# Optimization experiments

Hardware: AMD Instinct MI355X
Metric: run time of the kernel (lower is better)

## Reference

```python
import jax, jax.numpy as jnp
import numpy as np

N, E, L, H, C, F, NCLASS, NGRAPH = 50000, 800000, 3, 2, 64, 128, 10, 64
NEG_SLOPE = 0.2


def setup_inputs() -> dict:
    key = jax.random.key(0)
    ks = jax.random.split(key, 8)
    x = jax.random.normal(ks[0], (N, F), dtype=jnp.float32)
    edge_index = jax.random.randint(ks[1], (2, E), 0, N, dtype=jnp.int64)
    batch = jnp.sort(jax.random.randint(ks[2], (N,), 0, NGRAPH, dtype=jnp.int64))
    s = 1.0 / np.sqrt(F)
    W = jax.random.normal(ks[3], (L, F, H * C), dtype=jnp.float32) * s
    att_src = jax.random.normal(ks[4], (L, H, C), dtype=jnp.float32) * s
    att_dst = jax.random.normal(ks[5], (L, H, C), dtype=jnp.float32) * s
    bias = jnp.zeros((L, H * C), dtype=jnp.float32)
    lin_w = jax.random.normal(ks[6], (H * C, NCLASS), dtype=jnp.float32) * s
    lin_b = jnp.zeros((NCLASS,), dtype=jnp.float32)
    return {"x": x, "edge_index": edge_index, "batch": batch, "W": W,
            "att_src": att_src, "att_dst": att_dst, "bias": bias,
            "lin_w": lin_w, "lin_b": lin_b}


def _gat_layer(x, src, dst, w, a_s, a_d, b):
    n = x.shape[0]
    h = (x @ w).reshape(n, H, C)                      # [N,H,C]
    alpha_src = jnp.sum(h * a_s, axis=-1)             # [N,H]
    alpha_dst = jnp.sum(h * a_d, axis=-1)             # [N,H]
    e = jax.nn.leaky_relu(alpha_src[src] + alpha_dst[dst], NEG_SLOPE)  # [E2,H]
    # scatter-softmax over incoming edges of each destination node
    m = jax.ops.segment_max(e, dst, num_segments=n)
    p = jnp.exp(e - m[dst])
    z = jax.ops.segment_sum(p, dst, num_segments=n)
    alpha = p / z[dst]                                # [E2,H]
    msg = h[src] * alpha[:, :, None]                  # [E2,H,C]
    out = jax.ops.segment_sum(msg, dst, num_segments=n)  # [N,H,C]
    return out.reshape(n, H * C) + b


def reference(x, edge_index, batch, W, att_src, att_dst, bias, lin_w, lin_b):
    n = x.shape[0]
    # PyG GATConv default: add self-loops
    loop = jnp.arange(n, dtype=edge_index.dtype)
    src = jnp.concatenate([edge_index[0], loop])
    dst = jnp.concatenate([edge_index[1], loop])
    for l in range(L):
        x = _gat_layer(x, src, dst, W[l], att_src[l], att_dst[l], bias[l])
        x = jax.nn.elu(x)  # activation; dropout/bn inactive (eval, use_bn=False)
    # global mean pool per graph
    sums = jax.ops.segment_sum(x, batch, num_segments=NGRAPH)
    cnt = jax.ops.segment_sum(jnp.ones((n,), x.dtype), batch, num_segments=NGRAPH)
    pooled = sums / jnp.maximum(cnt, 1.0)[:, None]    # [NGRAPH, H*C]
    logits = pooled @ lin_w + lin_b
    return jax.nn.softmax(logits, axis=1)
```

## Files before the change

### kernel.cpp

```cpp
#include <hip/hip_runtime.h>
#include <math.h>

#define NNODES 50000
#define NEDGES 800000
#define NLAYERS 3
#define NHEADS 2
#define NCH 64
#define FDIM 128
#define NCLS 10
#define NGRAPH 64
#define NEG_SLOPE 0.2f
#define GEMMB ((NNODES + 63) / 64)
#define NB 391
#define RADB 391
#define SCN (NB * RADB)
#define NS1 ((SCN + 511) / 512)
#define PCH 8

#define WAVE_SYNC()                      \
  do {                                   \
    __builtin_amdgcn_wave_barrier();     \
    __asm__ volatile("" ::: "memory");   \
  } while (0)

typedef __attribute__((ext_vector_type(8))) short bf16x8;
typedef __attribute__((ext_vector_type(4))) float f32x4;

__device__ __forceinline__ unsigned short f2bf(float f) {
  unsigned int u = __builtin_bit_cast(unsigned int, f);
  unsigned int r = u + 0x7FFFu + ((u >> 16) & 1u);
  return (unsigned short)(r >> 16);
}
__device__ __forceinline__ float bflo(unsigned v) {
  return __builtin_bit_cast(float, v << 16);
}
__device__ __forceinline__ float bfhi(unsigned v) {
  return __builtin_bit_cast(float, v & 0xFFFF0000u);
}

__global__ __launch_bounds__(256) void k_wprep(const float* __restrict__ W,
                                               unsigned* __restrict__ Wt) {
  __shared__ float Lt[128][132];
  int l = blockIdx.x;
  const float* Wl = W + (size_t)l * FDIM * FDIM;
  unsigned* Wtl = Wt + (size_t)l * FDIM * FDIM / 2;
  int t = threadIdx.x;
#pragma unroll
  for (int i = 0; i < 16; ++i) {
    int k = (t >> 5) + 8 * i;
    int n4 = (t & 31) * 4;
    float4 v = *(const float4*)(Wl + (size_t)k * 128 + n4);
    Lt[k][n4 + 0] = v.x;
    Lt[k][n4 + 1] = v.y;
    Lt[k][n4 + 2] = v.z;
    Lt[k][n4 + 3] = v.w;
  }
  __syncthreads();
  int n = t >> 1;
  int kh = (t & 1) * 64;
  for (int kk = 0; kk < 64; kk += 2) {
    unsigned pk = (unsigned)f2bf(Lt[kh + kk][n]) |
                  ((unsigned)f2bf(Lt[kh + kk + 1][n]) << 16);
    Wtl[n * 64 + (kh >> 1) + (kk >> 1)] = pk;
  }
}

__global__ __launch_bounds__(128) void k_goff(const int* __restrict__ batch,
                                              int* __restrict__ goff,
                                              float* __restrict__ gsum) {
  int t = threadIdx.x;
  if (t < NGRAPH) {
    int lo = 0, hi = NNODES;
    while (lo < hi) {
      int mid = (lo + hi) >> 1;
      if (batch[mid] < t) lo = mid + 1;
      else hi = mid;
    }
    goff[t] = lo;
  }
  if (t == 0) goff[NGRAPH] = NNODES;
  for (int i = t; i < NGRAPH * FDIM; i += 128) gsum[i] = 0.f;
}

__device__ __forceinline__ void gemm_body(int blk, const float* __restrict__ X,
                                          const unsigned* __restrict__ Wt,
                                          const float* __restrict__ a_sL,
                                          const float* __restrict__ a_dL,
                                          unsigned* __restrict__ Hb,
                                          float* __restrict__ as_,
                                          float* __restrict__ ad_) {
  int t = threadIdx.x;
  int lane = t & 63;
  int w = t >> 6;
  int row0 = blk * 64;
  int n16 = lane & 15;
  int quad = lane >> 4;
  int m0 = w * 16;

  int gr = row0 + m0 + n16;
  const float* xp = X + (size_t)min(gr, NNODES - 1) * 128;

  f32x4 acc[8];
#pragma unroll
  for (int nt = 0; nt < 8; ++nt) {
    f32x4 z = {0.f, 0.f, 0.f, 0.f};
    acc[nt] = z;
  }
#pragma unroll
  for (int kk = 0; kk < 4; ++kk) {
    float4 va = *(const float4*)(xp + kk * 32 + quad * 8);
    float4 vb = *(const float4*)(xp + kk * 32 + quad * 8 + 4);
    bf16x8 af;
    af[0] = (short)f2bf(va.x); af[1] = (short)f2bf(va.y);
    af[2] = (short)f2bf(va.z); af[3] = (short)f2bf(va.w);
    af[4] = (short)f2bf(vb.x); af[5] = (short)f2bf(vb.y);
    af[6] = (short)f2bf(vb.z); af[7] = (short)f2bf(vb.w);
#pragma unroll
    for (int nt = 0; nt < 8; ++nt) {
      bf16x8 bf = *(const bf16x8*)(Wt + (size_t)(nt * 16 + n16) * 64 +
                                   kk * 16 + quad * 4);
      acc[nt] =
          __builtin_amdgcn_mfma_f32_16x16x32_bf16(af, bf, acc[nt], 0, 0, 0);
    }
  }

  float asv[8], adv[8];
#pragma unroll
  for (int nt = 0; nt < 8; ++nt) {
    asv[nt] = a_sL[nt * 16 + n16];
    adv[nt] = a_dL[nt * 16 + n16];
  }
#pragma unroll
  for (int r = 0; r < 4; ++r) {
    int row = row0 + m0 + quad * 4 + r;
    bool ok = (row < NNODES);
    float ps0 = 0.f, pd0 = 0.f, ps1 = 0.f, pd1 = 0.f;
#pragma unroll
    for (int nt = 0; nt < 4; ++nt) {
      ps0 += acc[nt][r] * asv[nt];
      pd0 += acc[nt][r] * adv[nt];
      ps1 += acc[nt + 4][r] * asv[nt + 4];
      pd1 += acc[nt + 4][r] * adv[nt + 4];
    }
#pragma unroll
    for (int off = 1; off < 16; off <<= 1) {
      ps0 += __shfl_xor(ps0, off, 64);
      pd0 += __shfl_xor(pd0, off, 64);
      ps1 += __shfl_xor(ps1, off, 64);
      pd1 += __shfl_xor(pd1, off, 64);
    }
    if (ok && n16 == 0) {
      as_[row * 2 + 0] = ps0;
      as_[row * 2 + 1] = ps1;
      ad_[row * 2 + 0] = pd0;
      ad_[row * 2 + 1] = pd1;
    }
    if (ok) {
#pragma unroll
      for (int nt = 0; nt < 4; ++nt) {
        unsigned pk = (unsigned)f2bf(acc[nt][r]) |
                      ((unsigned)f2bf(acc[nt + 4][r]) << 16);
        Hb[(size_t)row * 64 + nt * 16 + n16] = pk;
      }
    }
  }
}

__global__ __launch_bounds__(256) void k_gemm(const float* __restrict__ X,
                                              const unsigned* __restrict__ Wt,
                                              const float* __restrict__ a_sL,
                                              const float* __restrict__ a_dL,
                                              unsigned* __restrict__ Hb,
                                              float* __restrict__ as_,
                                              float* __restrict__ ad_) {
  gemm_body(blockIdx.x, X, Wt, a_sL, a_dL, Hb, as_, ad_);
}

__global__ __launch_bounds__(256) void k_front(
    const float* __restrict__ X, const unsigned* __restrict__ Wt,
    const float* __restrict__ a_sL, const float* __restrict__ a_dL,
    unsigned* __restrict__ Hb, float* __restrict__ as_,
    float* __restrict__ ad_, const int* __restrict__ ei,
    int* __restrict__ bh) {
  int b = blockIdx.x;
  if (b < GEMMB) {
    gemm_body(b, X, Wt, a_sL, a_dL, Hb, as_, ad_);
  } else {
    __shared__ int hist[NB];
    int blk = b - GEMMB;
    int t = threadIdx.x;
    for (int i = t; i < NB; i += 256) hist[i] = 0;
    __syncthreads();
    int e0 = blk * 2048;
#pragma unroll
    for (int i = 0; i < 8; ++i) {
      int e = e0 + i * 256 + t;
      if (e < NEDGES) atomicAdd(&hist[ei[NEDGES + e] >> 7], 1);
    }
    __syncthreads();
    for (int i = t; i < NB; i += 256) bh[i * RADB + blk] = hist[i];
  }
}

__global__ __launch_bounds__(256) void k_s1(int* __restrict__ sc,
                                            int* __restrict__ bpart) {
  __shared__ int ps[256];
  int t = threadIdx.x;
  int f0 = blockIdx.x * 512 + 2 * t;
  int x0 = (f0 < SCN) ? sc[f0] : 0;
  int x1 = (f0 + 1 < SCN) ? sc[f0 + 1] : 0;
  int pair = x0 + x1;
  ps[t] = pair;
  __syncthreads();
  for (int off = 1; off < 256; off <<= 1) {
    int v = (t >= off) ? ps[t - off] : 0;
    __syncthreads();
    ps[t] += v;
    __syncthreads();
  }
  int ex = ps[t] - pair;
  if (f0 < SCN) sc[f0] = ex;
  if (f0 + 1 < SCN) sc[f0 + 1] = ex + x0;
  if (t == 255) bpart[blockIdx.x] = ps[255];
}

__global__ __launch_bounds__(256) void k_s2(int* __restrict__ bpart) {
  __shared__ int ps[256];
  int t = threadIdx.x;
  int x0 = (2 * t < NS1) ? bpart[2 * t] : 0;
  int x1 = (2 * t + 1 < NS1) ? bpart[2 * t + 1] : 0;
  int pair = x0 + x1;
  ps[t] = pair;
  __syncthreads();
  for (int off = 1; off < 256; off <<= 1) {
    int v = (t >= off) ? ps[t - off] : 0;
    __syncthreads();
    ps[t] += v;
    __syncthreads();
  }
  int ex = ps[t] - pair;
  if (2 * t < NS1) bpart[2 * t] = ex;
  if (2 * t + 1 < NS1) bpart[2 * t + 1] = ex + x0;
}

__global__ __launch_bounds__(256) void k_s3(int* __restrict__ sc,
                                            const int* __restrict__ bpart) {
  int t = threadIdx.x;
  int f0 = blockIdx.x * 512 + 2 * t;
  int add = bpart[blockIdx.x];
  if (f0 < SCN) sc[f0] += add;
  if (f0 + 1 < SCN) sc[f0 + 1] += add;
}

__global__ __launch_bounds__(256) void k_passB(const int* __restrict__ ei,
                                               const int* __restrict__ sc,
                                               unsigned* __restrict__ ebuf) {
  __shared__ int curs[NB];
  int blk = blockIdx.x, t = threadIdx.x;
  for (int i = t; i < NB; i += 256) curs[i] = sc[i * RADB + blk];
  __syncthreads();
  int e0 = blk * 2048;
#pragma unroll
  for (int i = 0; i < 8; ++i) {
    int e = e0 + i * 256 + t;
    if (e < NEDGES) {
      int s = ei[e];
      int d = ei[NEDGES + e];
      int pos = atomicAdd(&curs[d >> 7], 1);
      ebuf[pos] = ((unsigned)s << 7) | (unsigned)(d & 127);
    }
  }
}

__global__ __launch_bounds__(256) void k_passC(const unsigned* __restrict__ ebuf,
                                               const int* __restrict__ sc,
                                               int* __restrict__ row_ptr,
                                               int* __restrict__ csr) {
  __shared__ int deg[128];
  __shared__ int scn[128];
  int b = blockIdx.x, t = threadIdx.x;
  int node0 = b * 128;
  int nn = min(128, NNODES - node0);
  int estart = sc[b * RADB];
  int eend = (b + 1 < NB) ? sc[(b + 1) * RADB] : NEDGES;
  if (t < 128) deg[t] = 0;
  __syncthreads();
  for (int e = estart + t; e < eend; e += 256)
    atomicAdd(&deg[ebuf[e] & 127], 1);
  __syncthreads();
  if (t < 128) scn[t] = (t < nn) ? deg[t] + 1 : 0;
  __syncthreads();
  for (int off = 1; off < 128; off <<= 1) {
    int v = (t < 128 && t >= off) ? scn[t - off] : 0;
    __syncthreads();
    if (t < 128) scn[t] += v;
    __syncthreads();
  }
  int base = estart + node0;
  if (t < nn) {
    int st = base + (t ? scn[t - 1] : 0);
    row_ptr[node0 + t] = st;
    csr[st] = node0 + t;
    deg[t] = st + 1;
  }
  if (b == 0 && t == 0) row_ptr[NNODES] = NEDGES + NNODES;
  __syncthreads();
  for (int e = estart + t; e < eend; e += 256) {
    unsigned v = ebuf[e];
    int pos = atomicAdd(&deg[v & 127], 1);
    csr[pos] = (int)(v >> 7);
  }
}

__global__ __launch_bounds__(256) void k_aggregate(
    const unsigned* __restrict__ Hb, const float* __restrict__ as_,
    const float* __restrict__ ad_, const int* __restrict__ row_ptr,
    const int* __restrict__ csr, const float* __restrict__ bias,
    float* __restrict__ Xout) {
  __shared__ float2 wb[4][64];
  __shared__ int sb[4][64];
  int wv = threadIdx.x >> 6;
  int lane = threadIdx.x & 63;
  int node = blockIdx.x * 4 + wv;
  if (node >= NNODES) return;
  int rs = row_ptr[node], re = row_ptr[node + 1];
  float2 adv = *(const float2*)&ad_[node * 2];
  const unsigned* Hl = Hb + lane;

  float z0 = 0.f, z1 = 0.f, acc0 = 0.f, acc1 = 0.f;
  for (int base = rs; base < re; base += 64) {
    int j = base + lane;
    float p0 = 0.f, p1 = 0.f;
    int s = 0;
    if (j < re) {
      s = csr[j];
      float2 asv = *(const float2*)&as_[s * 2];
      float e0 = asv.x + adv.x; e0 = (e0 > 0.f) ? e0 : NEG_SLOPE * e0;
      float e1 = asv.y + adv.y; e1 = (e1 > 0.f) ? e1 : NEG_SLOPE * e1;
      p0 = __expf(e0);
      p1 = __expf(e1);
    }
    z0 += p0;
    z1 += p1;
    wb[wv][lane] = make_float2(p0, p1);
    sb[wv][lane] = s;
    WAVE_SYNC();
    int cl = min(64, re - base);
    int jj = 0;
    for (; jj + 8 <= cl; jj += 8) {
      unsigned v0 = Hl[(size_t)sb[wv][jj + 0] * 64];
      unsigned v1 = Hl[(size_t)sb[wv][jj + 1] * 64];
      unsigned v2 = Hl[(size_t)sb[wv][jj + 2] * 64];
      unsigned v3 = Hl[(size_t)sb[wv][jj + 3] * 64];
      unsigned v4 = Hl[(size_t)sb[wv][jj + 4] * 64];
      unsigned v5 = Hl[(size_t)sb[wv][jj + 5] * 64];
      unsigned v6 = Hl[(size_t)sb[wv][jj + 6] * 64];
      unsigned v7 = Hl[(size_t)sb[wv][jj + 7] * 64];
      float2 w0 = wb[wv][jj + 0], w1 = wb[wv][jj + 1];
      float2 w2 = wb[wv][jj + 2], w3 = wb[wv][jj + 3];
      float2 w4 = wb[wv][jj + 4], w5 = wb[wv][jj + 5];
      float2 w6 = wb[wv][jj + 6], w7 = wb[wv][jj + 7];
      acc0 += w0.x * bflo(v0); acc1 += w0.y * bfhi(v0);
      acc0 += w1.x * bflo(v1); acc1 += w1.y * bfhi(v1);
      acc0 += w2.x * bflo(v2); acc1 += w2.y * bfhi(v2);
      acc0 += w3.x * bflo(v3); acc1 += w3.y * bfhi(v3);
      acc0 += w4.x * bflo(v4); acc1 += w4.y * bfhi(v4);
      acc0 += w5.x * bflo(v5); acc1 += w5.y * bfhi(v5);
      acc0 += w6.x * bflo(v6); acc1 += w6.y * bfhi(v6);
      acc0 += w7.x * bflo(v7); acc1 += w7.y * bfhi(v7);
    }
    for (; jj < cl; ++jj) {
      unsigned v = Hl[(size_t)sb[wv][jj] * 64];
      float2 w = wb[wv][jj];
      acc0 += w.x * bflo(v);
      acc1 += w.y * bfhi(v);
    }
    WAVE_SYNC();
  }
#pragma unroll
  for (int off = 32; off > 0; off >>= 1) {
    z0 += __shfl_xor(z0, off, 64);
    z1 += __shfl_xor(z1, off, 64);
  }
  float o0 = acc0 / z0 + bias[lane];
  float o1 = acc1 / z1 + bias[64 + lane];
  o0 = (o0 > 0.f) ? o0 : expm1f(o0);
  o1 = (o1 > 0.f) ? o1 : expm1f(o1);
  Xout[(size_t)node * 128 + lane] = o0;
  Xout[(size_t)node * 128 + 64 + lane] = o1;
}

__global__ __launch_bounds__(256) void k_pool2(const float* __restrict__ Xf,
                                               const int* __restrict__ goff,
                                               float* __restrict__ gsum) {
  __shared__ float red[128];
  int b = blockIdx.x;
  int g = b >> 3, ch = b & 7;
  int t = threadIdx.x;
  int c = t & 127, rh = t >> 7;
  int s = goff[g], e = goff[g + 1];
  int len = e - s;
  int c0 = s + (len * ch) / PCH;
  int c1 = s + (len * (ch + 1)) / PCH;
  float acc = 0.f;
  for (int n = c0 + rh; n < c1; n += 2) acc += Xf[(size_t)n * 128 + c];
  if (rh) red[c] = acc;
  __syncthreads();
  if (!rh) atomicAdd(&gsum[g * FDIM + c], acc + red[c]);
}

__global__ __launch_bounds__(64) void k_final(const float* __restrict__ gsum,
                                              const int* __restrict__ goff,
                                              const float* __restrict__ lw,
                                              const float* __restrict__ lb,
                                              float* __restrict__ out) {
  int g = threadIdx.x;
  float cnt = (float)(goff[g + 1] - goff[g]);
  float inv = 1.f / fmaxf(cnt, 1.f);
  float lg[NCLS];
#pragma unroll
  for (int k = 0; k < NCLS; ++k) lg[k] = lb[k];
  for (int c = 0; c < FDIM; ++c) {
    float pv = gsum[g * FDIM + c] * inv;
#pragma unroll
    for (int k = 0; k < NCLS; ++k) lg[k] += pv * lw[c * NCLS + k];
  }
  float mx = lg[0];
#pragma unroll
  for (int k = 1; k < NCLS; ++k) mx = fmaxf(mx, lg[k]);
  float s = 0.f;
#pragma unroll
  for (int k = 0; k < NCLS; ++k) {
    lg[k] = expf(lg[k] - mx);
    s += lg[k];
  }
  float invs = 1.f / s;
#pragma unroll
  for (int k = 0; k < NCLS; ++k) out[g * NCLS + k] = lg[k] * invs;
}


extern "C" void kernel_launch(void* const* d_in, const int* in_sizes, int n_in,
                              void* d_out, int out_size, void* d_ws,
                              size_t ws_size, hipStream_t stream) {
  const float* x = (const float*)d_in[0];
  const int* ei = (const int*)d_in[1];
  const int* batch = (const int*)d_in[2];
  const float* W = (const float*)d_in[3];
  const float* a_s = (const float*)d_in[4];
  const float* a_d = (const float*)d_in[5];
  const float* bias = (const float*)d_in[6];
  const float* lw = (const float*)d_in[7];
  const float* lb = (const float*)d_in[8];
  float* out = (float*)d_out;

  unsigned* Hb = (unsigned*)d_ws;
  float* xb = (float*)(Hb + (size_t)NNODES * 64);
  float* as_ = xb + (size_t)NNODES * 128;
  float* ad_ = as_ + (size_t)NNODES * 2;
  float* gsum = ad_ + (size_t)NNODES * 2;
  int* goff = (int*)(gsum + NGRAPH * FDIM);
  int* row_ptr = goff + (NGRAPH + 1);
  int* csr = row_ptr + (NNODES + 1);
  int* sc = csr + (NEDGES + NNODES);
  int* bpart = sc + SCN;
  unsigned* ebuf = (unsigned*)(bpart + NS1);
  unsigned* Wt = ebuf + (NEDGES + 1024);

  k_wprep<<<NLAYERS, 256, 0, stream>>>(W, Wt);
  k_goff<<<1, 128, 0, stream>>>(batch, goff, gsum);
  k_front<<<GEMMB + RADB, 256, 0, stream>>>(x, Wt, a_s, a_d, Hb, as_, ad_, ei,
                                            sc);
  k_s1<<<NS1, 256, 0, stream>>>(sc, bpart);
  k_s2<<<1, 256, 0, stream>>>(bpart);
  k_s3<<<NS1, 256, 0, stream>>>(sc, bpart);
  k_passB<<<RADB, 256, 0, stream>>>(ei, sc, ebuf);
  k_passC<<<NB, 256, 0, stream>>>(ebuf, sc, row_ptr, csr);

  for (int l = 0; l < NLAYERS; ++l) {
    if (l > 0) {
      k_gemm<<<GEMMB, 256, 0, stream>>>(xb, Wt + (size_t)l * FDIM * FDIM / 2,
                                        a_s + l * FDIM, a_d + l * FDIM, Hb,
                                        as_, ad_);
    }
    k_aggregate<<<(NNODES + 3) / 4, 256, 0, stream>>>(
        Hb, as_, ad_, row_ptr, csr, bias + l * FDIM, xb);
  }
  k_pool2<<<NGRAPH * PCH, 256, 0, stream>>>(xb, goff, gsum);
  k_final<<<1, 64, 0, stream>>>(gsum, goff, lw, lb, out);
}
```

Before: 324.2 us.

## Replace 3-kernel radix scan with atomic bucket offsets; vectorize aggregate FMAs

Each histogram block now reserves its per-bucket offset with a global atomicAdd on a bucket counter. Only the 391 bucket totals need a single-block scan, which replaces the three-kernel scan over 391x391 entries and removes two launches plus the large scan traffic. The aggregate kernel's scalar accumulators become four float2 vector accumulators, allowing packed FMA and more independent accumulation chains. Edge order within a bucket becomes nondeterministic because of the atomics, but the CSR result stays correct since passC rebuilds it per node. The changed accumulation order can slightly alter floating-point rounding.

After: 334.4 us. +3.1%, slower.

```diff
diff --git a/kernel.cpp b/kernel.cpp
--- a/kernel.cpp
+++ b/kernel.cpp
@@ -13,8 +13,6 @@
 #define GEMMB ((NNODES + 63) / 64)
 #define NB 391
 #define RADB 391
-#define SCN (NB * RADB)
-#define NS1 ((SCN + 511) / 512)
 #define PCH 8
 
 #define WAVE_SYNC()                      \
@@ -25,6 +23,7 @@
 
 typedef __attribute__((ext_vector_type(8))) short bf16x8;
 typedef __attribute__((ext_vector_type(4))) float f32x4;
+typedef __attribute__((ext_vector_type(2))) float f32x2;
 
 __device__ __forceinline__ unsigned short f2bf(float f) {
   unsigned int u = __builtin_bit_cast(unsigned int, f);
@@ -67,7 +66,8 @@
 
 __global__ __launch_bounds__(128) void k_goff(const int* __restrict__ batch,
                                               int* __restrict__ goff,
-                                              float* __restrict__ gsum) {
+                                              float* __restrict__ gsum,
+                                              int* __restrict__ bcnt) {
   int t = threadIdx.x;
   if (t < NGRAPH) {
     int lo = 0, hi = NNODES;
@@ -80,6 +80,7 @@
   }
   if (t == 0) goff[NGRAPH] = NNODES;
   for (int i = t; i < NGRAPH * FDIM; i += 128) gsum[i] = 0.f;
+  for (int i = t; i < NB; i += 128) bcnt[i] = 0;
 }
 
 __device__ __forceinline__ void gemm_body(int blk, const float* __restrict__ X,
@@ -180,8 +181,8 @@
     const float* __restrict__ X, const unsigned* __restrict__ Wt,
     const float* __restrict__ a_sL, const float* __restrict__ a_dL,
     unsigned* __restrict__ Hb, float* __restrict__ as_,
-    float* __restrict__ ad_, const int* __restrict__ ei,
-    int* __restrict__ bh) {
+    float* __restrict__ ad_, const int* __restrict__ ei, int* __restrict__ bh,
+    int* __restrict__ bcnt) {
   int b = blockIdx.x;
   if (b < GEMMB) {
     gemm_body(b, X, Wt, a_sL, a_dL, Hb, as_, ad_);
@@ -198,17 +199,20 @@
       if (e < NEDGES) atomicAdd(&hist[ei[NEDGES + e] >> 7], 1);
     }
     __syncthreads();
-    for (int i = t; i < NB; i += 256) bh[i * RADB + blk] = hist[i];
-  }
-}
-
-__global__ __launch_bounds__(256) void k_s1(int* __restrict__ sc,
-                                            int* __restrict__ bpart) {
+    for (int i = t; i < NB; i += 256) {
+      int c = hist[i];
+      int base = c ? atomicAdd(&bcnt[i], c) : 0;
+      bh[i * RADB + blk] = base;
+    }
+  }
+}
+
+__global__ __launch_bounds__(256) void k_bscan(const int* __restrict__ bcnt,
+                                               int* __restrict__ bstart) {
   __shared__ int ps[256];
   int t = threadIdx.x;
-  int f0 = blockIdx.x * 512 + 2 * t;
-  int x0 = (f0 < SCN) ? sc[f0] : 0;
-  int x1 = (f0 + 1 < SCN) ? sc[f0 + 1] : 0;
+  int x0 = (2 * t < NB) ? bcnt[2 * t] : 0;
+  int x1 = (2 * t + 1 < NB) ? bcnt[2 * t + 1] : 0;
   int pair = x0 + x1;
   ps[t] = pair;
   __syncthreads();
@@ -219,45 +223,18 @@
     __syncthreads();
   }
   int ex = ps[t] - pair;
-  if (f0 < SCN) sc[f0] = ex;
-  if (f0 + 1 < SCN) sc[f0 + 1] = ex + x0;
-  if (t == 255) bpart[blockIdx.x] = ps[255];
-}
-
-__global__ __launch_bounds__(256) void k_s2(int* __restrict__ bpart) {
-  __shared__ int ps[256];
-  int t = threadIdx.x;
-  int x0 = (2 * t < NS1) ? bpart[2 * t] : 0;
-  int x1 = (2 * t + 1 < NS1) ? bpart[2 * t + 1] : 0;
-  int pair = x0 + x1;
-  ps[t] = pair;
-  __syncthreads();
-  for (int off = 1; off < 256; off <<= 1) {
-    int v = (t >= off) ? ps[t - off] : 0;
-    __syncthreads();
-    ps[t] += v;
-    __syncthreads();
-  }
-  int ex = ps[t] - pair;
-  if (2 * t < NS1) bpart[2 * t] = ex;
-  if (2 * t + 1 < NS1) bpart[2 * t + 1] = ex + x0;
-}
-
-__global__ __launch_bounds__(256) void k_s3(int* __restrict__ sc,
-                                            const int* __restrict__ bpart) {
-  int t = threadIdx.x;
-  int f0 = blockIdx.x * 512 + 2 * t;
-  int add = bpart[blockIdx.x];
-  if (f0 < SCN) sc[f0] += add;
-  if (f0 + 1 < SCN) sc[f0 + 1] += add;
+  if (2 * t < NB) bstart[2 * t] = ex;
+  if (2 * t + 1 < NB) bstart[2 * t + 1] = ex + x0;
+  if (t == 0) bstart[NB] = NEDGES;
 }
 
 __global__ __launch_bounds__(256) void k_passB(const int* __restrict__ ei,
-                                               const int* __restrict__ sc,
+                                               const int* __restrict__ bstart,
+                                               const int* __restrict__ bh,
                                                unsigned* __restrict__ ebuf) {
   __shared__ int curs[NB];
   int blk = blockIdx.x, t = threadIdx.x;
-  for (int i = t; i < NB; i += 256) curs[i] = sc[i * RADB + blk];
+  for (int i = t; i < NB; i += 256) curs[i] = bstart[i] + bh[i * RADB + blk];
   __syncthreads();
   int e0 = blk * 2048;
 #pragma unroll
@@ -273,7 +250,7 @@
 }
 
 __global__ __launch_bounds__(256) void k_passC(const unsigned* __restrict__ ebuf,
-                                               const int* __restrict__ sc,
+                                               const int* __restrict__ bstart,
                                                int* __restrict__ row_ptr,
                                                int* __restrict__ csr) {
   __shared__ int deg[128];
@@ -281,8 +258,8 @@
   int b = blockIdx.x, t = threadIdx.x;
   int node0 = b * 128;
   int nn = min(128, NNODES - node0);
-  int estart = sc[b * RADB];
-  int eend = (b + 1 < NB) ? sc[(b + 1) * RADB] : NEDGES;
+  int estart = bstart[b];
+  int eend = bstart[b + 1];
   if (t < 128) deg[t] = 0;
   __syncthreads();
   for (int e = estart + t; e < eend; e += 256)
@@ -317,7 +294,7 @@
     const float* __restrict__ ad_, const int* __restrict__ row_ptr,
     const int* __restrict__ csr, const float* __restrict__ bias,
     float* __restrict__ Xout) {
-  __shared__ float2 wb[4][64];
+  __shared__ f32x2 wb[4][64];
   __shared__ int sb[4][64];
   int wv = threadIdx.x >> 6;
   int lane = threadIdx.x & 63;
@@ -327,7 +304,8 @@
   float2 adv = *(const float2*)&ad_[node * 2];
   const unsigned* Hl = Hb + lane;
 
-  float z0 = 0.f, z1 = 0.f, acc0 = 0.f, acc1 = 0.f;
+  float z0 = 0.f, z1 = 0.f;
+  f32x2 A0 = {0.f, 0.f}, A1 = {0.f, 0.f}, A2 = {0.f, 0.f}, A3 = {0.f, 0.f};
   for (int base = rs; base < re; base += 64) {
     int j = base + lane;
     float p0 = 0.f, p1 = 0.f;
@@ -342,7 +320,8 @@
     }
     z0 += p0;
     z1 += p1;
-    wb[wv][lane] = make_float2(p0, p1);
+    f32x2 pp = {p0, p1};
+    wb[wv][lane] = pp;
     sb[wv][lane] = s;
     WAVE_SYNC();
     int cl = min(64, re - base);
@@ -356,34 +335,43 @@
       unsigned v5 = Hl[(size_t)sb[wv][jj + 5] * 64];
       unsigned v6 = Hl[(size_t)sb[wv][jj + 6] * 64];
       unsigned v7 = Hl[(size_t)sb[wv][jj + 7] * 64];
-      float2 w0 = wb[wv][jj + 0], w1 = wb[wv][jj + 1];
-      float2 w2 = wb[wv][jj + 2], w3 = wb[wv][jj + 3];
-      float2 w4 = wb[wv][jj + 4], w5 = wb[wv][jj + 5];
-      float2 w6 = wb[wv][jj + 6], w7 = wb[wv][jj + 7];
-      acc0 += w0.x * bflo(v0); acc1 += w0.y * bfhi(v0);
-      acc0 += w1.x * bflo(v1); acc1 += w1.y * bfhi(v1);
-      acc0 += w2.x * bflo(v2); acc1 += w2.y * bfhi(v2);
-      acc0 += w3.x * bflo(v3); acc1 += w3.y * bfhi(v3);
-      acc0 += w4.x * bflo(v4); acc1 += w4.y * bfhi(v4);
-      acc0 += w5.x * bflo(v5); acc1 += w5.y * bfhi(v5);
-      acc0 += w6.x * bflo(v6); acc1 += w6.y * bfhi(v6);
-      acc0 += w7.x * bflo(v7); acc1 += w7.y * bfhi(v7);
+      f32x2 w0 = wb[wv][jj + 0], w1 = wb[wv][jj + 1];
+      f32x2 w2 = wb[wv][jj + 2], w3 = wb[wv][jj + 3];
+      f32x2 w4 = wb[wv][jj + 4], w5 = wb[wv][jj + 5];
+      f32x2 w6 = wb[wv][jj + 6], w7 = wb[wv][jj + 7];
+      f32x2 h0 = {bflo(v0), bfhi(v0)};
+      f32x2 h1 = {bflo(v1), bfhi(v1)};
+      f32x2 h2 = {bflo(v2), bfhi(v2)};
+      f32x2 h3 = {bflo(v3), bfhi(v3)};
+      f32x2 h4 = {bflo(v4), bfhi(v4)};
+      f32x2 h5 = {bflo(v5), bfhi(v5)};
+      f32x2 h6 = {bflo(v6), bfhi(v6)};
+      f32x2 h7 = {bflo(v7), bfhi(v7)};
+      A0 = h0 * w0 + A0;
+      A1 = h1 * w1 + A1;
+      A2 = h2 * w2 + A2;
+      A3 = h3 * w3 + A3;
+      A0 = h4 * w4 + A0;
+      A1 = h5 * w5 + A1;
+      A2 = h6 * w6 + A2;
+      A3 = h7 * w7 + A3;
     }
     for (; jj < cl; ++jj) {
       unsigned v = Hl[(size_t)sb[wv][jj] * 64];
-      float2 w = wb[wv][jj];
-      acc0 += w.x * bflo(v);
-      acc1 += w.y * bfhi(v);
+      f32x2 w = wb[wv][jj];
+      f32x2 h = {bflo(v), bfhi(v)};
+      A0 = h * w + A0;
     }
     WAVE_SYNC();
   }
+  f32x2 A = (A0 + A1) + (A2 + A3);
 #pragma unroll
   for (int off = 32; off > 0; off >>= 1) {
     z0 += __shfl_xor(z0, off, 64);
     z1 += __shfl_xor(z1, off, 64);
   }
-  float o0 = acc0 / z0 + bias[lane];
-  float o1 = acc1 / z1 + bias[64 + lane];
+  float o0 = A.x / z0 + bias[lane];
+  float o1 = A.y / z1 + bias[64 + lane];
   o0 = (o0 > 0.f) ? o0 : expm1f(o0);
   o1 = (o1 > 0.f) ? o1 : expm1f(o1);
   Xout[(size_t)node * 128 + lane] = o0;
@@ -460,22 +448,21 @@
   float* ad_ = as_ + (size_t)NNODES * 2;
   float* gsum = ad_ + (size_t)NNODES * 2;
   int* goff = (int*)(gsum + NGRAPH * FDIM);
-  int* row_ptr = goff + (NGRAPH + 1);
+  int* bcnt = goff + (NGRAPH + 1);
+  int* bstart = bcnt + NB;
+  int* row_ptr = bstart + (NB + 1);
   int* csr = row_ptr + (NNODES + 1);
-  int* sc = csr + (NEDGES + NNODES);
-  int* bpart = sc + SCN;
-  unsigned* ebuf = (unsigned*)(bpart + NS1);
+  int* bh = csr + (NEDGES + NNODES);
+  unsigned* ebuf = (unsigned*)(bh + NB * RADB);
   unsigned* Wt = ebuf + (NEDGES + 1024);
 
   k_wprep<<<NLAYERS, 256, 0, stream>>>(W, Wt);
-  k_goff<<<1, 128, 0, stream>>>(batch, goff, gsum);
+  k_goff<<<1, 128, 0, stream>>>(batch, goff, gsum, bcnt);
   k_front<<<GEMMB + RADB, 256, 0, stream>>>(x, Wt, a_s, a_d, Hb, as_, ad_, ei,
-                                            sc);
-  k_s1<<<NS1, 256, 0, stream>>>(sc, bpart);
-  k_s2<<<1, 256, 0, stream>>>(bpart);
-  k_s3<<<NS1, 256, 0, stream>>>(sc, bpart);
-  k_passB<<<RADB, 256, 0, stream>>>(ei, sc, ebuf);
-  k_passC<<<NB, 256, 0, stream>>>(ebuf, sc, row_ptr, csr);
+                                            bh, bcnt);
+  k_bscan<<<1, 256, 0, stream>>>(bcnt, bstart);
+  k_passB<<<RADB, 256, 0, stream>>>(ei, bstart, bh, ebuf);
+  k_passC<<<NB, 256, 0, stream>>>(ebuf, bstart, row_ptr, csr);
 
   for (int l = 0; l < NLAYERS; ++l) {
     if (l > 0) {
```
